# Kernel optimization log

Hardware: AMD Instinct MI355X
Metric: run time of the kernel (lower is better)

The kernel has to match this reference:

```python
import jax, jax.numpy as jnp
import numpy as np

EPS = 1e-8  # torch F.cosine_similarity eps


def setup_inputs() -> dict:
    key = jax.random.key(0)
    x = jax.random.normal(key, (16, 256, 2048), dtype=jnp.float32)
    return {"x": x}


def reference(x) -> jnp.ndarray:
    # x: [b, c, p]. Pairwise cosine similarity between point columns, diag = 1.
    # Equivalent to the original O(p) loop of F.cosine_similarity calls,
    # fused into one batched matmul.
    b, c, p = x.shape
    dots = jnp.einsum("bcp,bcq->bpq", x, x)            # [b, p, p]
    norms = jnp.sqrt(jnp.sum(x * x, axis=1))            # [b, p]
    denom = jnp.maximum(norms[:, :, None] * norms[:, None, :], EPS)
    sim = dots / denom
    eye = jnp.eye(p, dtype=x.dtype)
    res = jnp.where(eye[None, :, :] > 0, jnp.ones((), x.dtype), sim)
    return res
```

## Files before the change

### kernel.cpp

```cpp
#include <hip/hip_runtime.h>

#define B_ 16
#define C_ 256
#define P_ 2048
#define BK 32
#define NT 136
#define NT_OFF 120

typedef __attribute__((ext_vector_type(8))) short short8;
typedef __attribute__((ext_vector_type(4))) float floatx4;

__device__ inline short f2bf(float v) {
  union { float f; unsigned u; } c; c.f = v;
  unsigned r = c.u + 0x7fffu + ((c.u >> 16) & 1u);
  return (short)(r >> 16);
}

#define GLOAD_LDS16(g, l)                                          \
  __builtin_amdgcn_global_load_lds(                                \
      (const __attribute__((address_space(1))) void*)(g),          \
      (__attribute__((address_space(3))) void*)(l), 16, 0, 0)

__global__ void k_transpose(const float* __restrict__ x, short* __restrict__ Xt,
                            float* __restrict__ nrm2) {
  __shared__ float t[32][33];
  __shared__ float red[8][32];
  const int p0 = blockIdx.x * 32, c0 = blockIdx.y * 32, b = blockIdx.z;
  const float* xb = x + (size_t)b * C_ * P_;
  short* xtb = Xt + (size_t)b * P_ * C_;
  const int tx = threadIdx.x, ty = threadIdx.y;
  float s = 0.f;
#pragma unroll
  for (int i = 0; i < 4; ++i) {
    float v = xb[(size_t)(c0 + ty + i * 8) * P_ + p0 + tx];
    t[ty + i * 8][tx] = v;
    s += v * v;
  }
  red[ty][tx] = s;
  __syncthreads();
  const int tid = ty * 32 + tx;
  const int r = tid >> 3, ch = tid & 7;
  short4 v;
  v.x = f2bf(t[ch * 4 + 0][r]);
  v.y = f2bf(t[ch * 4 + 1][r]);
  v.z = f2bf(t[ch * 4 + 2][r]);
  v.w = f2bf(t[ch * 4 + 3][r]);
  *reinterpret_cast<short4*>(&xtb[(size_t)(p0 + r) * C_ + c0 + ch * 4]) = v;
  if (tid < 32) {
    float ns = 0.f;
#pragma unroll
    for (int j = 0; j < 8; ++j) ns += red[j][tid];
    atomicAdd(&nrm2[b * P_ + p0 + tid], ns);
  }
}

__global__ __launch_bounds__(256, 3) void k_gemm(const short* __restrict__ Xt,
                                                 const float* __restrict__ nrm2,
                                                 float* __restrict__ out) {
  const int bid = blockIdx.x;
  const int xcd = bid & 7;
  const int s = bid >> 3;
  const int b = xcd * 2 + (s >= NT);
  int t = s - (s >= NT ? NT : 0);

  int tm, tn;
  if (t < NT_OFF) {
    int rem = t, len = 15;
    tm = 0;
    while (rem >= len) { rem -= len; --len; ++tm; }
    tn = tm + 1 + rem;
  } else {
    tm = tn = t - NT_OFF;
  }
  const int p0 = tm * 128, q0 = tn * 128;
  const short* Xb = Xt + (size_t)b * P_ * C_;

  __shared__ __align__(16) char smem[32768];
  __shared__ __align__(16) float etile_s[4 * 1280];

  const int tid = threadIdx.x;
  const int lane = tid & 63;
  const int wid = tid >> 6;
  const int wrow = wid >> 1;
  const int wcol = wid & 1;

  floatx4 acc[4][4];
#pragma unroll
  for (int i = 0; i < 4; ++i)
#pragma unroll
    for (int j = 0; j < 4; ++j) acc[i][j] = (floatx4){0.f, 0.f, 0.f, 0.f};

  const int K2 = C_ * 2;

  auto STAGE = [&](int buf, int kt) {
    const int kb = kt * (BK * 2);
#pragma unroll
    for (int j = 0; j < 2; ++j) {
      const int chunk = j * 4 + wid;
      const int f = chunk * 1024 + lane * 16;
      const int row = f >> 6;
      const int inrow = f & 63;
      GLOAD_LDS16((const char*)Xb + (size_t)(p0 + row) * K2 + kb + inrow,
                  smem + buf * 8192 + chunk * 1024);
      GLOAD_LDS16((const char*)Xb + (size_t)(q0 + row) * K2 + kb + inrow,
                  smem + 16384 + buf * 8192 + chunk * 1024);
    }
  };

  STAGE(0, 0);

  for (int kt = 0; kt < C_ / BK; ++kt) {
    const int cur = kt & 1;
    if (kt < C_ / BK - 1) {
      STAGE(cur ^ 1, kt + 1);
      asm volatile("s_waitcnt vmcnt(4)\n\ts_barrier" ::: "memory");
    } else {
      asm volatile("s_waitcnt vmcnt(0)\n\ts_barrier" ::: "memory");
    }

    const short* As = (const short*)(smem + cur * 8192);
    const short* Bs = (const short*)(smem + 16384 + cur * 8192);
    short8 af[4], bf[4];
#pragma unroll
    for (int mi = 0; mi < 4; ++mi) {
      const int r = wrow * 64 + mi * 16 + (lane & 15);
      af[mi] = *reinterpret_cast<const short8*>(&As[r * BK + (lane >> 4) * 8]);
    }
#pragma unroll
    for (int ni = 0; ni < 4; ++ni) {
      const int r = wcol * 64 + ni * 16 + (lane & 15);
      bf[ni] = *reinterpret_cast<const short8*>(&Bs[r * BK + (lane >> 4) * 8]);
    }
#pragma unroll
    for (int mi = 0; mi < 4; ++mi)
#pragma unroll
      for (int ni = 0; ni < 4; ++ni)
        acc[mi][ni] = __builtin_amdgcn_mfma_f32_16x16x32_bf16(af[mi], bf[ni], acc[mi][ni], 0, 0, 0);

    asm volatile("s_waitcnt lgkmcnt(0)\n\ts_barrier" ::: "memory");
  }

  const float* n2 = nrm2 + (size_t)b * P_;
  float* ob = out + (size_t)b * P_ * P_;
  const int cl = lane & 15, rg4 = (lane >> 4) * 4;

  float rnq[4];
#pragma unroll
  for (int ni = 0; ni < 4; ++ni) {
    const int qc = q0 + wcol * 64 + ni * 16 + cl;
    rnq[ni] = __builtin_amdgcn_rcpf(fmaxf(sqrtf(n2[qc]), 1e-4f));
  }
  floatx4 rnp[4];
#pragma unroll
  for (int mi = 0; mi < 4; ++mi) {
    const float4 p2 = *reinterpret_cast<const float4*>(&n2[p0 + wrow * 64 + mi * 16 + rg4]);
    rnp[mi][0] = __builtin_amdgcn_rcpf(fmaxf(sqrtf(p2.x), 1e-4f));
    rnp[mi][1] = __builtin_amdgcn_rcpf(fmaxf(sqrtf(p2.y), 1e-4f));
    rnp[mi][2] = __builtin_amdgcn_rcpf(fmaxf(sqrtf(p2.z), 1e-4f));
    rnp[mi][3] = __builtin_amdgcn_rcpf(fmaxf(sqrtf(p2.w), 1e-4f));
  }

  float* etile = etile_s + wid * 1280;

#pragma unroll
  for (int mi = 0; mi < 4; ++mi) {
    const int prow = p0 + wrow * 64 + mi * 16 + rg4;
#pragma unroll
    for (int ni = 0; ni < 4; ++ni) {
      floatx4 vv = acc[mi][ni] * rnp[mi] * rnq[ni];
      const int qc = q0 + wcol * 64 + ni * 16 + cl;
      if (tm == tn) {
        const int d = qc - prow;
        if (d >= 0 && d < 4) vv[d] = 1.0f;
      }
      ob[(size_t)(prow + 0) * P_ + qc] = vv[0];
      ob[(size_t)(prow + 1) * P_ + qc] = vv[1];
      ob[(size_t)(prow + 2) * P_ + qc] = vv[2];
      ob[(size_t)(prow + 3) * P_ + qc] = vv[3];
      if (tm != tn)
        *reinterpret_cast<floatx4*>(&etile[(ni * 16 + cl) * 20 + rg4]) = vv;
    }
    if (tm != tn) {
      const int pcb = p0 + wrow * 64 + mi * 16;
#pragma unroll
      for (int i = 0; i < 4; ++i) {
        const int qq = i * 16 + (lane >> 2);
        const floatx4 mv = *reinterpret_cast<const floatx4*>(&etile[qq * 20 + (lane & 3) * 4]);
        *reinterpret_cast<floatx4*>(
            &ob[(size_t)(q0 + wcol * 64 + qq) * P_ + pcb + (lane & 3) * 4]) = mv;
      }
    }
  }
}

extern "C" void kernel_launch(void* const* d_in, const int* in_sizes, int n_in,
                              void* d_out, int out_size, void* d_ws, size_t ws_size,
                              hipStream_t stream) {
  const float* x = (const float*)d_in[0];
  float* out = (float*)d_out;

  short* Xt = (short*)d_ws;
  float* nrm2 = (float*)((char*)d_ws + (size_t)B_ * P_ * C_ * sizeof(short));

  hipMemsetAsync(nrm2, 0, (size_t)B_ * P_ * sizeof(float), stream);
  k_transpose<<<dim3(P_ / 32, C_ / 32, B_), dim3(32, 8), 0, stream>>>(x, Xt, nrm2);
  k_gemm<<<dim3(NT * B_), 256, 0, stream>>>(Xt, nrm2, out);
}
```

Before: 90.75 us.

## Loop transpose over channels, drop norm atomics and memset, alias epilogue LDS

The transpose kernel now has each block loop over all channel chunks of a 32-point slab. This lets it accumulate the squared norm locally and store it directly, so the memset launch and the atomics go away, at the cost of fewer blocks with more serial work each. The GEMM reuses its staging shared memory for the epilogue transpose tile instead of a separate buffer. Cutting LDS this way allows launch bounds of 4 blocks per CU, and the pipeline wait now moves to the end of each iteration.

```diff
diff --git a/kernel.cpp b/kernel.cpp
--- a/kernel.cpp
+++ b/kernel.cpp
@@ -21,40 +21,47 @@
       (const __attribute__((address_space(1))) void*)(g),          \
       (__attribute__((address_space(3))) void*)(l), 16, 0, 0)
 
-__global__ void k_transpose(const float* __restrict__ x, short* __restrict__ Xt,
-                            float* __restrict__ nrm2) {
+__global__ __launch_bounds__(256, 4) void k_transpose(const float* __restrict__ x,
+                                                      short* __restrict__ Xt,
+                                                      float* __restrict__ nrm2) {
   __shared__ float t[32][33];
   __shared__ float red[8][32];
-  const int p0 = blockIdx.x * 32, c0 = blockIdx.y * 32, b = blockIdx.z;
+  const int p0 = blockIdx.x * 32, b = blockIdx.y;
   const float* xb = x + (size_t)b * C_ * P_;
   short* xtb = Xt + (size_t)b * P_ * C_;
   const int tx = threadIdx.x, ty = threadIdx.y;
+  const int tid = ty * 32 + tx;
+  const int r = tid >> 3, ch = tid & 7;
   float s = 0.f;
-#pragma unroll
-  for (int i = 0; i < 4; ++i) {
-    float v = xb[(size_t)(c0 + ty + i * 8) * P_ + p0 + tx];
-    t[ty + i * 8][tx] = v;
-    s += v * v;
+#pragma unroll 1
+  for (int ci = 0; ci < 8; ++ci) {
+    const int c0 = ci * 32;
+#pragma unroll
+    for (int i = 0; i < 4; ++i) {
+      float v = xb[(size_t)(c0 + ty + i * 8) * P_ + p0 + tx];
+      t[ty + i * 8][tx] = v;
+      s += v * v;
+    }
+    __syncthreads();
+    short4 w;
+    w.x = f2bf(t[ch * 4 + 0][r]);
+    w.y = f2bf(t[ch * 4 + 1][r]);
+    w.z = f2bf(t[ch * 4 + 2][r]);
+    w.w = f2bf(t[ch * 4 + 3][r]);
+    *reinterpret_cast<short4*>(&xtb[(size_t)(p0 + r) * C_ + c0 + ch * 4]) = w;
+    __syncthreads();
   }
   red[ty][tx] = s;
   __syncthreads();
-  const int tid = ty * 32 + tx;
-  const int r = tid >> 3, ch = tid & 7;
-  short4 v;
-  v.x = f2bf(t[ch * 4 + 0][r]);
-  v.y = f2bf(t[ch * 4 + 1][r]);
-  v.z = f2bf(t[ch * 4 + 2][r]);
-  v.w = f2bf(t[ch * 4 + 3][r]);
-  *reinterpret_cast<short4*>(&xtb[(size_t)(p0 + r) * C_ + c0 + ch * 4]) = v;
   if (tid < 32) {
     float ns = 0.f;
 #pragma unroll
     for (int j = 0; j < 8; ++j) ns += red[j][tid];
-    atomicAdd(&nrm2[b * P_ + p0 + tid], ns);
-  }
-}
-
-__global__ __launch_bounds__(256, 3) void k_gemm(const short* __restrict__ Xt,
+    nrm2[b * P_ + p0 + tid] = ns;
+  }
+}
+
+__global__ __launch_bounds__(256, 4) void k_gemm(const short* __restrict__ Xt,
                                                  const float* __restrict__ nrm2,
                                                  float* __restrict__ out) {
   const int bid = blockIdx.x;
@@ -76,7 +83,6 @@
   const short* Xb = Xt + (size_t)b * P_ * C_;
 
   __shared__ __align__(16) char smem[32768];
-  __shared__ __align__(16) float etile_s[4 * 1280];
 
   const int tid = threadIdx.x;
   const int lane = tid & 63;
@@ -108,15 +114,11 @@
   };
 
   STAGE(0, 0);
+  asm volatile("s_waitcnt vmcnt(0)\n\ts_barrier" ::: "memory");
 
   for (int kt = 0; kt < C_ / BK; ++kt) {
     const int cur = kt & 1;
-    if (kt < C_ / BK - 1) {
-      STAGE(cur ^ 1, kt + 1);
-      asm volatile("s_waitcnt vmcnt(4)\n\ts_barrier" ::: "memory");
-    } else {
-      asm volatile("s_waitcnt vmcnt(0)\n\ts_barrier" ::: "memory");
-    }
+    if (kt < C_ / BK - 1) STAGE(cur ^ 1, kt + 1);
 
     const short* As = (const short*)(smem + cur * 8192);
     const short* Bs = (const short*)(smem + 16384 + cur * 8192);
@@ -137,7 +139,7 @@
       for (int ni = 0; ni < 4; ++ni)
         acc[mi][ni] = __builtin_amdgcn_mfma_f32_16x16x32_bf16(af[mi], bf[ni], acc[mi][ni], 0, 0, 0);
 
-    asm volatile("s_waitcnt lgkmcnt(0)\n\ts_barrier" ::: "memory");
+    asm volatile("s_waitcnt vmcnt(0) lgkmcnt(0)\n\ts_barrier" ::: "memory");
   }
 
   const float* n2 = nrm2 + (size_t)b * P_;
@@ -160,7 +162,7 @@
     rnp[mi][3] = __builtin_amdgcn_rcpf(fmaxf(sqrtf(p2.w), 1e-4f));
   }
 
-  float* etile = etile_s + wid * 1280;
+  float* etile = (float*)smem + wid * 1280;
 
 #pragma unroll
   for (int mi = 0; mi < 4; ++mi) {
@@ -202,7 +204,6 @@
   short* Xt = (short*)d_ws;
   float* nrm2 = (float*)((char*)d_ws + (size_t)B_ * P_ * C_ * sizeof(short));
 
-  hipMemsetAsync(nrm2, 0, (size_t)B_ * P_ * sizeof(float), stream);
-  k_transpose<<<dim3(P_ / 32, C_ / 32, B_), dim3(32, 8), 0, stream>>>(x, Xt, nrm2);
+  k_transpose<<<dim3(P_ / 32, B_), dim3(32, 8), 0, stream>>>(x, Xt, nrm2);
   k_gemm<<<dim3(NT * B_), 256, 0, stream>>>(Xt, nrm2, out);
 }
```

Result: no change. 92.48 us (+1.9%).
